# Performance work log

Hardware: AMD Instinct MI355X
Metric: run time of the kernel (lower is better)

## Reference

```python
import jax, jax.numpy as jnp
import numpy as np
from jax import lax

B, CODELEN, COMLEN, NAST, SUBG = 32, 50, 30, 300, 4
EMB, H, ASTHOPS = 300, 256, 2
AST_VOCAB, COM_VOCAB = 10000, 10000


def gru(x, h0, wih, whh, bih, bhh):
    # PyTorch GRU cell semantics. x: [N, T, D], h0: [N, H] -> (ys [N,T,H], hT [N,H])
    xg = jnp.einsum('ntd,gd->ntg', x, wih) + bih  # precompute input gates [N,T,3H]
    def step(h, xt):
        hg = h @ whh.T + bhh
        xr, xz, xn = jnp.split(xt, 3, axis=-1)
        hr, hz, hn = jnp.split(hg, 3, axis=-1)
        r = jax.nn.sigmoid(xr + hr)
        z = jax.nn.sigmoid(xz + hz)
        n = jnp.tanh(xn + r * hn)
        hnew = (1.0 - z) * n + z * h
        return hnew, hnew
    hT, ys = lax.scan(step, h0, jnp.swapaxes(xg, 0, 1))
    return jnp.swapaxes(ys, 0, 1), hT


def dot_attn(q, k):
    # DotProductAttention in eval mode (dropout = identity)
    scale = 1.0 / jnp.sqrt(jnp.asarray(q.shape[-1], q.dtype))
    s = jnp.einsum('bqd,bkd->bqk', q, k) * scale
    return jnp.einsum('bqk,bkd->bqd', jax.nn.softmax(s, axis=-1), k)


def setup_inputs() -> dict:
    key = jax.random.key(0)
    ks = jax.random.split(key, 32)
    def rn(k, shp, sc=0.05):
        return jax.random.normal(k, shp, jnp.float32) * sc
    inp = {}
    inp['x0'] = jax.random.randint(ks[0], (B, CODELEN), 0, AST_VOCAB)
    inp['x1'] = jax.random.randint(ks[1], (B, COMLEN), 0, COM_VOCAB)
    inp['x2'] = jax.random.randint(ks[2], (B, SUBG, NAST), 0, AST_VOCAB)
    inp['adj'] = jax.random.uniform(ks[3], (B, SUBG, NAST, NAST), jnp.float32) * (1.0 / NAST)
    inp['emb_ast'] = rn(ks[4], (AST_VOCAB, EMB), 0.5)
    inp['emb_com'] = rn(ks[5], (COM_VOCAB, EMB), 0.5)
    inp['gru1_wih'] = rn(ks[6], (3 * H, EMB)); inp['gru1_whh'] = rn(ks[7], (3 * H, H))
    inp['gru1_bih'] = rn(ks[8], (3 * H,));    inp['gru1_bhh'] = rn(ks[9], (3 * H,))
    inp['gru2_wih'] = rn(ks[10], (3 * H, EMB)); inp['gru2_whh'] = rn(ks[11], (3 * H, H))
    inp['gru2_bih'] = rn(ks[12], (3 * H,));     inp['gru2_bhh'] = rn(ks[13], (3 * H,))
    inp['gru4_wih'] = rn(ks[14], (3 * H, NAST * EMB), 0.01)
    inp['gru4_whh'] = rn(ks[15], (3 * H, H))
    inp['gru4_bih'] = rn(ks[16], (3 * H,)); inp['gru4_bhh'] = rn(ks[17], (3 * H,))
    inp['gru58_wih'] = rn(ks[18], (SUBG, 3 * H, EMB)); inp['gru58_whh'] = rn(ks[19], (SUBG, 3 * H, H))
    inp['gru58_bih'] = rn(ks[20], (SUBG, 3 * H));      inp['gru58_bhh'] = rn(ks[21], (SUBG, 3 * H))
    inp['gcn_w'] = rn(ks[22], (EMB, EMB)); inp['gcn_b'] = rn(ks[23], (EMB,))
    inp['dense_w'] = rn(ks[24], (H, 3 * H)); inp['dense_b'] = rn(ks[25], (H,))
    inp['lin_w'] = rn(ks[26], (COM_VOCAB, COMLEN * H), 0.01); inp['lin_b'] = rn(ks[27], (COM_VOCAB,))
    return inp


def reference(x0, x1, x2, adj, emb_ast, emb_com,
              gru1_wih, gru1_whh, gru1_bih, gru1_bhh,
              gru2_wih, gru2_whh, gru2_bih, gru2_bhh,
              gru4_wih, gru4_whh, gru4_bih, gru4_bhh,
              gru58_wih, gru58_whh, gru58_bih, gru58_bhh,
              gcn_w, gcn_b, dense_w, dense_b, lin_w, lin_b):
    b = x0.shape[0]
    scale = 1.0 / jnp.sqrt(jnp.float32(H))
    # token encoder + comment decoder
    tencout, tstate = gru(emb_ast[x0], jnp.zeros((b, H), jnp.float32),
                          gru1_wih, gru1_whh, gru1_bih, gru1_bhh)
    decout, _ = gru(emb_com[x1], tstate, gru2_wih, gru2_whh, gru2_bih, gru2_bhh)
    tcontext = dot_attn(decout, tencout)
    # GCN over 4 sub-graphs (torch code mutates astwork in place -> tmp alias sees post-GCN feats)
    astwork = jnp.transpose(emb_ast[x2], (1, 0, 2, 3))  # [4,B,N,300]
    adjp = jnp.transpose(adj, (1, 0, 2, 3))             # [4,B,N,N]
    for _ in range(ASTHOPS):
        support = jnp.einsum('sbnd,de->sbne', astwork, gcn_w)
        astwork = jax.nn.relu(jnp.einsum('sbnm,sbme->sbne', adjp, support) + gcn_b)
    # TimeDistributed(gru4): batch = 4 sub-graphs, sequence = B, input = flattened node feats
    g4in = astwork.reshape(SUBG, b, NAST * EMB)
    g4out, _ = gru(g4in, jnp.zeros((SUBG, H), jnp.float32),
                   gru4_wih, gru4_whh, gru4_bih, gru4_bhh)
    astw = jnp.transpose(g4out, (1, 0, 2))  # [B,4,H]
    ahier = jax.nn.softmax(jnp.einsum('bqd,bsd->bqs', decout, astw) * scale, axis=-1)
    ahier_p = jnp.transpose(ahier, (2, 0, 1))  # [4,B,Q]
    # per-sub-graph node GRUs (gru5..gru8) vmapped over the sub-graph axis
    outs, _ = jax.vmap(gru, in_axes=(0, None, 0, 0, 0, 0))(
        astwork, tstate, gru58_wih, gru58_whh, gru58_bih, gru58_bhh)  # [4,B,N,H]
    sc = jax.nn.softmax(jnp.einsum('bqd,sbkd->sbqk', decout, outs) * scale, axis=-1)
    new_atten = sc * ahier_p[:, :, :, None]  # element_wise_mul with hierarchy weights
    acontext = jnp.einsum('sbqk,sbkd->bqd', new_atten, outs)  # bmm then sum over sub-graphs
    acontext = dot_attn(decout, acontext)
    context = jnp.concatenate([tcontext, decout, acontext], axis=-1)  # [B,Q,768]
    out = jax.nn.relu(context @ dense_w.T + dense_b)
    out = out.reshape(b, -1)  # [B, 7680]
    return out @ lin_w.T + lin_b  # [B, comvocab]
```

## Files before the change

### kernel.cpp

```cpp
#include <hip/hip_runtime.h>
#include <hip/hip_fp16.h>
#include <hip/hip_bf16.h>


typedef __attribute__((ext_vector_type(8))) short  bf16x8;
typedef __attribute__((ext_vector_type(4))) float  f32x4;

__device__ inline unsigned short f2bs(float f) {
  __hip_bfloat16 h = __float2bfloat16(f);
  unsigned short u; __builtin_memcpy(&u, &h, 2); return u;
}
__device__ inline float bs2f(unsigned short u) {
  unsigned v = (unsigned)u << 16;
  float f; __builtin_memcpy(&f, &v, 4); return f;
}
__device__ inline float sigf(float x) { return 1.f / (1.f + __expf(-x)); }
__device__ inline float tanhf_(float x) {
  const float e = __expf(-2.f * fabsf(x));
  return copysignf((1.f - e) / (1.f + e), x);
}

template <bool ABF, bool BBF, int OUTM, bool RELU, bool GATHER = false, bool BKN = false>
__global__ __launch_bounds__(256) void k_mfma(
    const void* __restrict__ Av, long lda, long a_ss, long a_sb,
    const void* __restrict__ Bv, long ldb, long b_ss, long b_sb,
    void* __restrict__ Cv, long ldc, long c_ss, long c_sb,
    const float* __restrict__ bias, long bias_ss,
    const int* __restrict__ gidx,
    int M, int N, int K, int zb, int ksplit)
{
  __shared__ unsigned short As[128][40];
  __shared__ unsigned short Bs[128][40];
  const int tid = threadIdx.x;
  const int zi = blockIdx.z;
  const int bi = zi / ksplit;
  const int ks = zi - bi * ksplit;
  const int sIdx = bi / zb;
  const int bIdx = bi - sIdx * zb;
  const int row0 = blockIdx.y * 128;
  const int col0 = blockIdx.x * 128;
  const int Kc = ((K + ksplit * 32 - 1) / (ksplit * 32)) * 32;
  const int kbeg = ks * Kc;
  const int kend = min(K, kbeg + Kc);
  if (kbeg >= kend) return;

  const char* Ab = (const char*)Av + ((long)sIdx * a_ss + (long)bIdx * a_sb) * (ABF ? 2 : 4);
  const char* Bb = (const char*)Bv + ((long)sIdx * b_ss + (long)bIdx * b_sb) * (BBF ? 2 : 4);
  char* Cb = (char*)Cv + ((long)sIdx * c_ss + (long)bIdx * c_sb) * ((OUTM == 1 || OUTM == 3) ? 2 : 4);

  const int w = tid >> 6, l = tid & 63;
  const int wr = w >> 1, wc = w & 1;
  const int lr = l & 15, lg = l >> 4;

  f32x4 acc[4][4];
#pragma unroll
  for (int m = 0; m < 4; ++m)
#pragma unroll
    for (int n = 0; n < 4; ++n) acc[m][n] = f32x4{0.f, 0.f, 0.f, 0.f};

  const int sr = tid >> 1;
  const int sk = (tid & 1) * 16;

  for (int kt = kbeg; kt < kend; kt += 32) {
    {
      const int gr = row0 + sr;
      if (ABF) {
        const unsigned short* src = (const unsigned short*)(Ab + ((long)gr * lda + kt + sk) * 2);
        if (gr < M && kt + sk + 16 <= kend) {
          const uint2* p = (const uint2*)src;
          *(uint2*)&As[sr][sk + 0]  = p[0];
          *(uint2*)&As[sr][sk + 4]  = p[1];
          *(uint2*)&As[sr][sk + 8]  = p[2];
          *(uint2*)&As[sr][sk + 12] = p[3];
        } else {
#pragma unroll
          for (int i = 0; i < 16; ++i) {
            const int kk = kt + sk + i;
            As[sr][sk + i] = (gr < M && kk < kend) ? src[i] : (unsigned short)0;
          }
        }
      } else {
        const float* src;
        if (GATHER) src = (const float*)Av + ((gr < M) ? (long)gidx[gr] * lda : 0) + kt + sk;
        else        src = (const float*)(Ab + ((long)gr * lda + kt + sk) * 4);
        if (gr < M && kt + sk + 16 <= kend) {
#pragma unroll
          for (int q = 0; q < 4; ++q) {
            const float4 v = ((const float4*)src)[q];
            *(unsigned*)&As[sr][sk + q * 4 + 0] = (unsigned)f2bs(v.x) | ((unsigned)f2bs(v.y) << 16);
            *(unsigned*)&As[sr][sk + q * 4 + 2] = (unsigned)f2bs(v.z) | ((unsigned)f2bs(v.w) << 16);
          }
        } else {
#pragma unroll
          for (int i = 0; i < 16; ++i) {
            const int kk = kt + sk + i;
            As[sr][sk + i] = (gr < M && kk < kend) ? f2bs(src[i]) : (unsigned short)0;
          }
        }
      }
    }
    if (BKN) {
      const int kk = tid >> 3;
      const int cb = (tid & 7) * 16;
      const int gk = kt + kk;
#pragma unroll
      for (int q = 0; q < 16; ++q) {
        const int gc = col0 + cb + q;
        unsigned short v = 0;
        if (gk < kend && gc < N) {
          if (BBF) v = ((const unsigned short*)Bb)[(long)gk * ldb + gc];
          else     v = f2bs(((const float*)Bb)[(long)gk * ldb + gc]);
        }
        Bs[cb + q][kk] = v;
      }
    } else {
      const int gc = col0 + sr;
      if (BBF) {
        const unsigned short* src = (const unsigned short*)(Bb + ((long)gc * ldb + kt + sk) * 2);
        if (gc < N && kt + sk + 16 <= kend) {
          const uint2* p = (const uint2*)src;
          *(uint2*)&Bs[sr][sk + 0]  = p[0];
          *(uint2*)&Bs[sr][sk + 4]  = p[1];
          *(uint2*)&Bs[sr][sk + 8]  = p[2];
          *(uint2*)&Bs[sr][sk + 12] = p[3];
        } else {
#pragma unroll
          for (int i = 0; i < 16; ++i) {
            const int kk = kt + sk + i;
            Bs[sr][sk + i] = (gc < N && kk < kend) ? src[i] : (unsigned short)0;
          }
        }
      } else {
        const float* src = (const float*)(Bb + ((long)gc * ldb + kt + sk) * 4);
        if (gc < N && kt + sk + 16 <= kend) {
#pragma unroll
          for (int q = 0; q < 4; ++q) {
            const float4 v = ((const float4*)src)[q];
            *(unsigned*)&Bs[sr][sk + q * 4 + 0] = (unsigned)f2bs(v.x) | ((unsigned)f2bs(v.y) << 16);
            *(unsigned*)&Bs[sr][sk + q * 4 + 2] = (unsigned)f2bs(v.z) | ((unsigned)f2bs(v.w) << 16);
          }
        } else {
#pragma unroll
          for (int i = 0; i < 16; ++i) {
            const int kk = kt + sk + i;
            Bs[sr][sk + i] = (gc < N && kk < kend) ? f2bs(src[i]) : (unsigned short)0;
          }
        }
      }
    }
    __syncthreads();
    bf16x8 af[4], bf[4];
#pragma unroll
    for (int m = 0; m < 4; ++m)
      af[m] = *(const bf16x8*)&As[wr * 64 + m * 16 + lr][lg * 8];
#pragma unroll
    for (int n = 0; n < 4; ++n)
      bf[n] = *(const bf16x8*)&Bs[wc * 64 + n * 16 + lr][lg * 8];
#pragma unroll
    for (int m = 0; m < 4; ++m)
#pragma unroll
      for (int n = 0; n < 4; ++n)
        acc[m][n] = __builtin_amdgcn_mfma_f32_16x16x32_bf16(af[m], bf[n], acc[m][n], 0, 0, 0);
    __syncthreads();
  }

  const float* bp = bias ? bias + (long)sIdx * bias_ss : nullptr;
#pragma unroll
  for (int m = 0; m < 4; ++m) {
#pragma unroll
    for (int n = 0; n < 4; ++n) {
      const int col = col0 + wc * 64 + n * 16 + lr;
      const int rb  = row0 + wr * 64 + m * 16 + lg * 4;
      const f32x4 v = acc[m][n];
      if (col >= N) continue;
      if (OUTM == 3) {
        unsigned short* ct = (unsigned short*)Cb + (long)col * ldc + rb;
        if (rb + 4 <= M) {
          ushort4 pk;
          pk.x = f2bs(v[0]); pk.y = f2bs(v[1]); pk.z = f2bs(v[2]); pk.w = f2bs(v[3]);
          *(ushort4*)ct = pk;
        } else {
#pragma unroll
          for (int r = 0; r < 4; ++r) if (rb + r < M) ct[r] = f2bs(v[r]);
        }
      } else {
        const float bv = bp ? bp[col] : 0.f;
#pragma unroll
        for (int r = 0; r < 4; ++r) {
          const int row = rb + r;
          if (row >= M) continue;
          float x = v[r] + bv;
          if (RELU) x = fmaxf(x, 0.f);
          if (OUTM == 0) ((float*)Cb)[(long)row * ldc + col] = x;
          else if (OUTM == 1) ((unsigned short*)Cb)[(long)row * ldc + col] = f2bs(x);
          else atomicAdd((float*)Cb + (long)row * ldc + col, x);
        }
      }
    }
  }
}

template <bool XBF, bool YBF>
__global__ __launch_bounds__(1024, 1) void k_gru_v3(
    const void* __restrict__ xg,
    const float* __restrict__ h0, int h0_mod,
    const unsigned short* __restrict__ whh_bf, long w_stride, int cpw,
    const float* __restrict__ bhh, long b_stride,
    void* __restrict__ ys, float* __restrict__ hT, int T)
{
  const int c   = blockIdx.x;
  const int tid = threadIdx.x;
  const int wv  = tid >> 6;
  const int l   = tid & 63;
  const int lr  = l & 15;
  const int lg  = l >> 4;

  __shared__ unsigned short A_lds[8][64][8];
  __shared__ float gate_lds[772];
  __shared__ float bhh_lds[768];
  __shared__ float h_lds[256];
  __shared__ uint4 xbuf[2][192];

  const unsigned short* W = whh_bf + (long)(c / cpw) * w_stride;
  bf16x8 bfr[3][8];
#pragma unroll
  for (int nt = 0; nt < 3; ++nt) {
    const unsigned short* wp = W + (long)(wv * 48 + nt * 16 + lr) * 256 + lg * 8;
#pragma unroll
    for (int kt = 0; kt < 8; ++kt)
      bfr[nt][kt] = *(const bf16x8*)(wp + kt * 32);
  }
  if (tid < 768) bhh_lds[tid] = bhh[(long)(c / cpw) * b_stride + tid];
  {
    unsigned* az = (unsigned*)A_lds;
    for (int i = tid; i < 2048; i += 1024) az[i] = 0;
  }
  __syncthreads();

  if (tid < 32) {
    const int j0 = tid * 8;
    bf16x8 pk;
#pragma unroll
    for (int e = 0; e < 8; ++e) {
      const float hv = h0 ? h0[(long)(c % h0_mod) * 256 + j0 + e] : 0.f;
      h_lds[j0 + e] = hv;
      pk[e] = (short)f2bs(hv);
    }
    *(bf16x8*)&A_lds[j0 >> 5][((j0 >> 3) & 3) * 16][0] = pk;
  }
  const int esz = XBF ? 2 : 4;
  const int xlanes = XBF ? 96 : 192;
  const char* xbase = (const char*)xg + (long)c * T * 768 * esz;
  if (tid < xlanes) xbuf[0][tid] = *(const uint4*)(xbase + tid * 16);
  __syncthreads();

  int cur = 0;
  for (int t = 0; t < T; ++t) {
    uint4 xs = uint4{0, 0, 0, 0};
    const bool xact = (tid < xlanes) && (t + 1 < T);
    if (xact) xs = *(const uint4*)(xbase + (long)(t + 1) * 768 * esz + tid * 16);

    f32x4 acc[3];
    acc[0] = f32x4{0.f, 0.f, 0.f, 0.f};
    acc[1] = f32x4{0.f, 0.f, 0.f, 0.f};
    acc[2] = f32x4{0.f, 0.f, 0.f, 0.f};
#pragma unroll
    for (int kt = 0; kt < 8; ++kt) {
      const bf16x8 af = *(const bf16x8*)&A_lds[kt][l][0];
#pragma unroll
      for (int nt = 0; nt < 3; ++nt)
        acc[nt] = __builtin_amdgcn_mfma_f32_16x16x32_bf16(af, bfr[nt][kt], acc[nt], 0, 0, 0);
    }
    if (lg == 0) {
#pragma unroll
      for (int nt = 0; nt < 3; ++nt)
        gate_lds[wv * 48 + nt * 16 + lr] = acc[nt][0];
    }
    __syncthreads();

    if (xact) xbuf[cur ^ 1][tid] = xs;

    if (tid < 32) {
      const int j0 = tid * 8;
      float hn[8];
#pragma unroll
      for (int e = 0; e < 8; ++e) {
        const int u = j0 + e;
        float xr, xz, xn;
        if (XBF) {
          const unsigned short* xp = (const unsigned short*)&xbuf[cur][0];
          xr = bs2f(xp[u]); xz = bs2f(xp[256 + u]); xn = bs2f(xp[512 + u]);
        } else {
          const float* xp = (const float*)&xbuf[cur][0];
          xr = xp[u]; xz = xp[256 + u]; xn = xp[512 + u];
        }
        const float rr = sigf(xr + gate_lds[u] + bhh_lds[u]);
        const float zz = sigf(xz + gate_lds[256 + u] + bhh_lds[256 + u]);
        const float nv = tanhf_(xn + rr * (gate_lds[512 + u] + bhh_lds[512 + u]));
        hn[e] = (1.f - zz) * nv + zz * h_lds[u];
      }
      bf16x8 pk;
#pragma unroll
      for (int e = 0; e < 8; ++e) {
        h_lds[j0 + e] = hn[e];
        pk[e] = (short)f2bs(hn[e]);
      }
      *(bf16x8*)&A_lds[j0 >> 5][((j0 >> 3) & 3) * 16][0] = pk;
      if (ys) {
        if (YBF) {
          unsigned short* yp = (unsigned short*)ys + ((long)c * T + t) * 256 + j0;
          *(bf16x8*)yp = pk;
        } else {
          float* yp = (float*)ys + ((long)c * T + t) * 256 + j0;
          *(float4*)yp = float4{hn[0], hn[1], hn[2], hn[3]};
          *(float4*)(yp + 4) = float4{hn[4], hn[5], hn[6], hn[7]};
        }
      }
    }
    __syncthreads();
    cur ^= 1;
  }
  if (hT && tid < 32) {
    const int j0 = tid * 8;
    float* hp = hT + (long)c * 256 + j0;
#pragma unroll
    for (int e = 0; e < 8; ++e) hp[e] = h_lds[j0 + e];
  }
}

__global__ __launch_bounds__(256) void k_init_bias(
    float* __restrict__ C, const float* __restrict__ bias, int M, int N)
{
  const int total = M * N;
  for (int i = blockIdx.x * 256 + threadIdx.x; i < total; i += gridDim.x * 256)
    C[i] = bias[i % N];
}

__global__ __launch_bounds__(256) void k_gather_ast(
    const float* __restrict__ emb, const int* __restrict__ x2,
    unsigned short* __restrict__ outp)
{
  const int total = 4 * 32 * 300 * 300;
  for (int idx = blockIdx.x * 256 + threadIdx.x; idx < total; idx += gridDim.x * 256) {
    const int d = idx % 300;
    const int r = idx / 300;
    const int n = r % 300;
    const int r2 = r / 300;
    const int b = r2 % 32;
    const int s = r2 / 32;
    outp[idx] = f2bs(emb[(long)x2[(b * 4 + s) * 300 + n] * 300 + d]);
  }
}

__global__ __launch_bounds__(256) void k_twb(
    const float* __restrict__ w, unsigned short* __restrict__ o, int R, int C)
{
  const int total = R * C;
  for (int i = blockIdx.x * 256 + threadIdx.x; i < total; i += gridDim.x * 256) {
    const int r = i / C, c = i - r * C;
    o[(long)c * R + r] = f2bs(w[i]);
  }
}

__global__ __launch_bounds__(256) void k_f2b(
    const float* __restrict__ a, unsigned short* __restrict__ o, int n)
{
  for (int i = blockIdx.x * 256 + threadIdx.x; i < n; i += gridDim.x * 256)
    o[i] = f2bs(a[i]);
}

__global__ __launch_bounds__(256) void k_attn(
    const float* __restrict__ q, const float* __restrict__ kv,
    float* __restrict__ out, int Q, int L)
{
  const int bq = blockIdx.x;
  const int b = bq / Q;
  const int tid = threadIdx.x;
  const int g = tid >> 3, l = tid & 7;
  __shared__ float qv[256];
  __shared__ float sc[64];
  qv[tid] = q[(long)bq * 256 + tid];
  __syncthreads();
  for (int k0 = 0; k0 < L; k0 += 32) {
    const int k = k0 + g;
    float s = 0.f;
    if (k < L) {
      const float* kr = kv + ((long)b * L + k) * 256;
      for (int d = l; d < 256; d += 8) s += qv[d] * kr[d];
    }
    s += __shfl_xor(s, 1);
    s += __shfl_xor(s, 2);
    s += __shfl_xor(s, 4);
    if (k < L && l == 0) sc[k] = s * 0.0625f;
  }
  __syncthreads();
  float m = -1e30f;
  for (int k = 0; k < L; ++k) m = fmaxf(m, sc[k]);
  float den = 0.f;
  for (int k = 0; k < L; ++k) den += __expf(sc[k] - m);
  __syncthreads();
  if (tid < L) sc[tid] = __expf(sc[tid] - m);
  __syncthreads();
  const float* kb = kv + (long)b * L * 256;
  float acc = 0.f;
  for (int k = 0; k < L; ++k) acc += sc[k] * kb[(long)k * 256 + tid];
  out[(long)bq * 256 + tid] = acc / den;
}

__global__ __launch_bounds__(64) void k_hier(
    const float* __restrict__ dec, const float* __restrict__ g4out,
    float* __restrict__ ahier, int Q)
{
  const int bq = blockIdx.x;
  const int b = bq / Q;
  const int l = threadIdx.x;
  float s[4] = {0.f, 0.f, 0.f, 0.f};
#pragma unroll
  for (int i = 0; i < 4; ++i) {
    const int d = l * 4 + i;
    const float qd = dec[(long)bq * 256 + d];
#pragma unroll
    for (int sg = 0; sg < 4; ++sg)
      s[sg] += qd * g4out[((long)sg * 32 + b) * 256 + d];
  }
#pragma unroll
  for (int off = 32; off >= 1; off >>= 1)
#pragma unroll
    for (int sg = 0; sg < 4; ++sg) s[sg] += __shfl_xor(s[sg], off);
  if (l == 0) {
    float m = -1e30f;
#pragma unroll
    for (int sg = 0; sg < 4; ++sg) m = fmaxf(m, s[sg] * 0.0625f);
    float e[4], den = 0.f;
#pragma unroll
    for (int sg = 0; sg < 4; ++sg) { e[sg] = __expf(s[sg] * 0.0625f - m); den += e[sg]; }
#pragma unroll
    for (int sg = 0; sg < 4; ++sg) ahier[(long)bq * 4 + sg] = e[sg] / den;
  }
}

__global__ __launch_bounds__(64) void k_smax(
    float* __restrict__ sc, const float* __restrict__ ahier)
{
  const int id = blockIdx.x;
  const int s = id / 960;
  const int bq = id - s * 960;
  float* row = sc + (long)id * 300;
  const int l = threadIdx.x;
  float v[5];
  float m = -1e30f;
#pragma unroll
  for (int i = 0; i < 5; ++i) {
    const int k = l + i * 64;
    v[i] = (k < 300) ? row[k] * 0.0625f : -1e30f;
    m = fmaxf(m, v[i]);
  }
#pragma unroll
  for (int off = 32; off >= 1; off >>= 1) m = fmaxf(m, __shfl_xor(m, off));
  float den = 0.f;
#pragma unroll
  for (int i = 0; i < 5; ++i) { v[i] = __expf(v[i] - m); den += v[i]; }
#pragma unroll
  for (int off = 32; off >= 1; off >>= 1) den += __shfl_xor(den, off);
  const float w = ahier[(long)bq * 4 + s] / den;
#pragma unroll
  for (int i = 0; i < 5; ++i) {
    const int k = l + i * 64;
    if (k < 300) row[k] = v[i] * w;
  }
}

__global__ __launch_bounds__(256) void k_concat(
    const float* __restrict__ a, const float* __restrict__ b,
    const float* __restrict__ c, float* __restrict__ out, int rows)
{
  const int total = rows * 768;
  for (int i = blockIdx.x * 256 + threadIdx.x; i < total; i += gridDim.x * 256) {
    const int r = i / 768, col = i - r * 768;
    float v;
    if (col < 256) v = a[(long)r * 256 + col];
    else if (col < 512) v = b[(long)r * 256 + col - 256];
    else v = c[(long)r * 256 + col - 512];
    out[i] = v;
  }
}

extern "C" void kernel_launch(void* const* d_in, const int* in_sizes, int n_in,
                              void* d_out, int out_size, void* d_ws, size_t ws_size,
                              hipStream_t stream) {
  const int*   x0      = (const int*)d_in[0];
  const int*   x1      = (const int*)d_in[1];
  const int*   x2      = (const int*)d_in[2];
  const float* adj     = (const float*)d_in[3];
  const float* emb_ast = (const float*)d_in[4];
  const float* emb_com = (const float*)d_in[5];
  const float* g1_wih  = (const float*)d_in[6];
  const float* g1_whh  = (const float*)d_in[7];
  const float* g1_bih  = (const float*)d_in[8];
  const float* g1_bhh  = (const float*)d_in[9];
  const float* g2_wih  = (const float*)d_in[10];
  const float* g2_whh  = (const float*)d_in[11];
  const float* g2_bih  = (const float*)d_in[12];
  const float* g2_bhh  = (const float*)d_in[13];
  const float* g4_wih  = (const float*)d_in[14];
  const float* g4_whh  = (const float*)d_in[15];
  const float* g4_bih  = (const float*)d_in[16];
  const float* g4_bhh  = (const float*)d_in[17];
  const float* g58_wih = (const float*)d_in[18];
  const float* g58_whh = (const float*)d_in[19];
  const float* g58_bih = (const float*)d_in[20];
  const float* g58_bhh = (const float*)d_in[21];
  const float* gcn_w   = (const float*)d_in[22];
  const float* gcn_b   = (const float*)d_in[23];
  const float* dw      = (const float*)d_in[24];
  const float* db      = (const float*)d_in[25];
  const float* lw      = (const float*)d_in[26];
  const float* lb      = (const float*)d_in[27];
  float* out = (float*)d_out;
  float* ws  = (float*)d_ws;

  unsigned short* astwork_bf = (unsigned short*)ws;
  unsigned short* supportT   = (unsigned short*)(ws + 5760000L);
  unsigned short* g58xg_bf   = (unsigned short*)(ws + 11520000L);
  unsigned short* outsb_bf   = (unsigned short*)(ws + 26265600L);
  unsigned short* xg1_bf     = (unsigned short*)(ws + 31180800L);
  unsigned short* xg2_bf     = (unsigned short*)(ws + 31795200L);
  float* tenc    = ws + 32163840L;
  float* tstate  = ws + 32573440L;
  float* dec     = ws + 32581632L;
  float* tctx    = ws + 32827392L;
  float* g4xg    = ws + 33073152L;
  float* g4out   = ws + 33171456L;
  float* ahier   = ws + 33204224L;
  float* actx1   = ws + 33208064L;
  float* actx    = ws + 33453824L;
  float* dense   = ws + 33699584L;
  float* ctmp    = ws + 33945344L;
  float* scbuf   = ws + 34682624L;
  unsigned short* gcn_wT    = (unsigned short*)(ws + 35834624L);
  unsigned short* dense_bf  = (unsigned short*)(ws + 35879624L);
  unsigned short* g1whh_bf  = (unsigned short*)(ws + 36002504L);
  unsigned short* g2whh_bf  = (unsigned short*)(ws + 36100808L);
  unsigned short* g4whh_bf  = (unsigned short*)(ws + 36199112L);
  unsigned short* g58whh_bf = (unsigned short*)(ws + 36297416L);

  const dim3 blk(256);

  k_gather_ast<<<dim3(4096), blk, 0, stream>>>(emb_ast, x2, astwork_bf);
  k_twb<<<dim3(90), blk, 0, stream>>>(gcn_w, gcn_wT, 300, 300);
  k_f2b<<<dim3(192), blk, 0, stream>>>(g1_whh, g1whh_bf, 196608);
  k_f2b<<<dim3(192), blk, 0, stream>>>(g2_whh, g2whh_bf, 196608);
  k_f2b<<<dim3(192), blk, 0, stream>>>(g4_whh, g4whh_bf, 196608);
  k_f2b<<<dim3(768), blk, 0, stream>>>(g58_whh, g58whh_bf, 786432);

  for (int hop = 0; hop < 2; ++hop) {
    k_mfma<true, true, 3, false><<<dim3(3, 3, 128), blk, 0, stream>>>(
        astwork_bf, 300, 2880000, 90000,
        gcn_wT, 300, 0, 0,
        supportT, 300, 2880000, 90000,
        nullptr, 0, nullptr, 300, 300, 300, 32, 1);
    k_mfma<false, true, 1, true><<<dim3(3, 3, 128), blk, 0, stream>>>(
        adj, 300, 90000, 360000,
        supportT, 300, 2880000, 90000,
        astwork_bf, 300, 2880000, 90000,
        gcn_b, 0, nullptr, 300, 300, 300, 32, 1);
  }

  k_mfma<false, false, 1, false, true><<<dim3(6, 13, 1), blk, 0, stream>>>(
      emb_ast, 300, 0, 0, g1_wih, 300, 0, 0, xg1_bf, 768, 0, 0,
      g1_bih, 0, x0, 1600, 768, 300, 1, 1);
  k_gru_v3<true, false><<<dim3(32), dim3(1024), 0, stream>>>(
      xg1_bf, nullptr, 1, g1whh_bf, 0, 32, g1_bhh, 0, tenc, tstate, 50);

  k_mfma<false, false, 1, false, true><<<dim3(6, 8, 1), blk, 0, stream>>>(
      emb_com, 300, 0, 0, g2_wih, 300, 0, 0, xg2_bf, 768, 0, 0,
      g2_bih, 0, x1, 960, 768, 300, 1, 1);
  k_gru_v3<true, false><<<dim3(32), dim3(1024), 0, stream>>>(
      xg2_bf, tstate, 32, g2whh_bf, 0, 32, g2_bhh, 0, dec, nullptr, 30);

  k_attn<<<dim3(960), blk, 0, stream>>>(dec, tenc, tctx, 30, 50);

  k_init_bias<<<dim3(384), blk, 0, stream>>>(g4xg, g4_bih, 128, 768);
  k_mfma<true, false, 2, false><<<dim3(6, 1, 43), blk, 0, stream>>>(
      astwork_bf, 90000, 0, 0, g4_wih, 90000, 0, 0, g4xg, 768, 0, 0,
      nullptr, 0, nullptr, 128, 768, 90000, 1, 43);
  k_gru_v3<false, false><<<dim3(4), dim3(1024), 0, stream>>>(
      g4xg, nullptr, 1, g4whh_bf, 0, 4, g4_bhh, 0, g4out, nullptr, 32);

  k_hier<<<dim3(960), dim3(64), 0, stream>>>(dec, g4out, ahier, 30);

  k_mfma<true, false, 1, false><<<dim3(6, 75, 4), blk, 0, stream>>>(
      astwork_bf, 300, 2880000, 0, g58_wih, 300, 230400, 0,
      g58xg_bf, 768, 7372800, 0, g58_bih, 768, nullptr, 9600, 768, 300, 1, 1);
  k_gru_v3<true, true><<<dim3(128), dim3(1024), 0, stream>>>(
      g58xg_bf, tstate, 32, g58whh_bf, 196608, 32, g58_bhh, 768,
      outsb_bf, nullptr, 300);

  k_mfma<false, true, 0, false><<<dim3(3, 1, 128), blk, 0, stream>>>(
      dec, 256, 0, 7680, outsb_bf, 256, 2457600, 76800, scbuf, 300, 288000, 9000,
      nullptr, 0, nullptr, 30, 300, 256, 32, 1);
  k_smax<<<dim3(3840), dim3(64), 0, stream>>>(scbuf, ahier);
  hipMemsetAsync(actx1, 0, 245760 * sizeof(float), stream);
  k_mfma<false, true, 2, false, false, true><<<dim3(2, 1, 128), blk, 0, stream>>>(
      scbuf, 300, 288000, 9000, outsb_bf, 256, 2457600, 76800, actx1, 256, 0, 7680,
      nullptr, 0, nullptr, 30, 256, 300, 32, 1);

  k_attn<<<dim3(960), blk, 0, stream>>>(dec, actx1, actx, 30, 30);

  k_concat<<<dim3(2880), blk, 0, stream>>>(tctx, dec, actx, ctmp, 960);
  k_mfma<false, false, 0, true><<<dim3(2, 8, 1), blk, 0, stream>>>(
      ctmp, 768, 0, 0, dw, 768, 0, 0, dense, 256, 0, 0,
      db, 0, nullptr, 960, 256, 768, 1, 1);
  k_f2b<<<dim3(960), blk, 0, stream>>>(dense, dense_bf, 245760);

  k_init_bias<<<dim3(1250), blk, 0, stream>>>(out, lb, 32, 10000);
  k_mfma<true, false, 2, false><<<dim3(79, 1, 6), blk, 0, stream>>>(
      dense_bf, 7680, 0, 0, lw, 7680, 0, 0, out, 10000, 0, 0,
      nullptr, 0, nullptr, 32, 10000, 7680, 1, 6);
}
```

Baseline: 1.893 ms.

## Batch multiple GRU chains per block and pre-convert adjacency to bf16

The GRU recurrence kernel now handles several independent sequences per block. They are stacked as rows of the MFMA A-operand, so one set of register-resident recurrent weights serves up to 16 chains at once, and the hidden state is kept in registers with double-buffered LDS. This cuts the grid from one block per sequence to a few blocks and replaces the near-empty 1-row MFMAs with fuller ones. It also reduces the per-step work of the single-thread-group gate update. Separately, the adjacency matrix is converted to bf16 once and then used in the GCN hops, which adds a conversion pass in exchange for halving A-operand traffic.

After: 2.303 ms. 21.6% more time.

```diff
diff --git a/kernel.cpp b/kernel.cpp
--- a/kernel.cpp
+++ b/kernel.cpp
@@ -200,131 +200,163 @@
   }
 }
 
-template <bool XBF, bool YBF>
-__global__ __launch_bounds__(1024, 1) void k_gru_v3(
+template <int CPB, bool XBF, bool YBF>
+__global__ __launch_bounds__(512) void k_gru_v4(
     const void* __restrict__ xg,
     const float* __restrict__ h0, int h0_mod,
     const unsigned short* __restrict__ whh_bf, long w_stride, int cpw,
     const float* __restrict__ bhh, long b_stride,
     void* __restrict__ ys, float* __restrict__ hT, int T)
 {
-  const int c   = blockIdx.x;
+  constexpr int ESZ  = XBF ? 2 : 4;
+  constexpr int VPR  = 768 * ESZ / 16;
+  constexpr int XVEC = CPB * VPR;
+  constexpr int NQ   = (XVEC + 511) / 512;
+
   const int tid = threadIdx.x;
+  const int c0  = blockIdx.x * CPB;
   const int wv  = tid >> 6;
   const int l   = tid & 63;
   const int lr  = l & 15;
   const int lg  = l >> 4;
 
-  __shared__ unsigned short A_lds[8][64][8];
-  __shared__ float gate_lds[772];
+  __shared__ unsigned short A_lds[2][8][64][8];
+  __shared__ float gate_lds[CPB][772];
   __shared__ float bhh_lds[768];
-  __shared__ float h_lds[256];
-  __shared__ uint4 xbuf[2][192];
-
-  const unsigned short* W = whh_bf + (long)(c / cpw) * w_stride;
-  bf16x8 bfr[3][8];
-#pragma unroll
-  for (int nt = 0; nt < 3; ++nt) {
-    const unsigned short* wp = W + (long)(wv * 48 + nt * 16 + lr) * 256 + lg * 8;
-#pragma unroll
-    for (int kt = 0; kt < 8; ++kt)
-      bfr[nt][kt] = *(const bf16x8*)(wp + kt * 32);
-  }
-  if (tid < 768) bhh_lds[tid] = bhh[(long)(c / cpw) * b_stride + tid];
-  {
-    unsigned* az = (unsigned*)A_lds;
-    for (int i = tid; i < 2048; i += 1024) az[i] = 0;
-  }
+  __shared__ uint4 xbuf[2][XVEC];
+
+  { unsigned* az = (unsigned*)A_lds;
+    for (int i = tid; i < 4096; i += 512) az[i] = 0; }
   __syncthreads();
 
-  if (tid < 32) {
-    const int j0 = tid * 8;
+  const unsigned short* W = whh_bf + (long)(c0 / cpw) * w_stride;
+  bf16x8 bfr[6][8];
+#pragma unroll
+  for (int nt = 0; nt < 6; ++nt) {
+    const unsigned short* wp = W + (long)(wv * 96 + nt * 16 + lr) * 256 + lg * 8;
+#pragma unroll
+    for (int kt = 0; kt < 8; ++kt) bfr[nt][kt] = *(const bf16x8*)(wp + kt * 32);
+  }
+  for (int i = tid; i < 768; i += 512)
+    bhh_lds[i] = bhh[(long)(c0 / cpw) * b_stride + i];
+
+  const int c   = tid >> 5;
+  const int jb  = tid & 31;
+  const bool act = c < CPB;
+  const int u0  = jb * 8;
+
+  float h[8];
+  if (act) {
+#pragma unroll
+    for (int e = 0; e < 8; ++e)
+      h[e] = h0 ? h0[(long)((c0 + c) % h0_mod) * 256 + u0 + e] : 0.f;
     bf16x8 pk;
 #pragma unroll
-    for (int e = 0; e < 8; ++e) {
-      const float hv = h0 ? h0[(long)(c % h0_mod) * 256 + j0 + e] : 0.f;
-      h_lds[j0 + e] = hv;
-      pk[e] = (short)f2bs(hv);
-    }
-    *(bf16x8*)&A_lds[j0 >> 5][((j0 >> 3) & 3) * 16][0] = pk;
-  }
-  const int esz = XBF ? 2 : 4;
-  const int xlanes = XBF ? 96 : 192;
-  const char* xbase = (const char*)xg + (long)c * T * 768 * esz;
-  if (tid < xlanes) xbuf[0][tid] = *(const uint4*)(xbase + tid * 16);
+    for (int e = 0; e < 8; ++e) pk[e] = (short)f2bs(h[e]);
+    *(bf16x8*)&A_lds[0][jb >> 2][(jb & 3) * 16 + c][0] = pk;
+  }
+
+  const char* xbase = (const char*)xg + (long)c0 * T * 768 * ESZ;
+  long poff[NQ]; bool pact[NQ];
+#pragma unroll
+  for (int q = 0; q < NQ; ++q) {
+    const int i = tid + q * 512;
+    pact[q] = i < XVEC;
+    const int ci = pact[q] ? i / VPR : 0;
+    const int of = i - ci * VPR;
+    poff[q] = (long)ci * T * 768 * ESZ + (long)of * 16;
+  }
+#pragma unroll
+  for (int q = 0; q < NQ; ++q)
+    if (pact[q]) ((uint4*)xbuf[0])[tid + q * 512] = *(const uint4*)(xbase + poff[q]);
   __syncthreads();
 
   int cur = 0;
   for (int t = 0; t < T; ++t) {
-    uint4 xs = uint4{0, 0, 0, 0};
-    const bool xact = (tid < xlanes) && (t + 1 < T);
-    if (xact) xs = *(const uint4*)(xbase + (long)(t + 1) * 768 * esz + tid * 16);
-
-    f32x4 acc[3];
-    acc[0] = f32x4{0.f, 0.f, 0.f, 0.f};
-    acc[1] = f32x4{0.f, 0.f, 0.f, 0.f};
-    acc[2] = f32x4{0.f, 0.f, 0.f, 0.f};
+    uint4 xs[NQ];
+    const bool pf = (t + 1 < T);
+    if (pf) {
+#pragma unroll
+      for (int q = 0; q < NQ; ++q)
+        if (pact[q]) xs[q] = *(const uint4*)(xbase + poff[q] + (long)(t + 1) * 768 * ESZ);
+    }
+
+    f32x4 acc[6];
+#pragma unroll
+    for (int nt = 0; nt < 6; ++nt) acc[nt] = f32x4{0.f, 0.f, 0.f, 0.f};
 #pragma unroll
     for (int kt = 0; kt < 8; ++kt) {
-      const bf16x8 af = *(const bf16x8*)&A_lds[kt][l][0];
-#pragma unroll
-      for (int nt = 0; nt < 3; ++nt)
+      const bf16x8 af = *(const bf16x8*)&A_lds[cur][kt][l][0];
+#pragma unroll
+      for (int nt = 0; nt < 6; ++nt)
         acc[nt] = __builtin_amdgcn_mfma_f32_16x16x32_bf16(af, bfr[nt][kt], acc[nt], 0, 0, 0);
     }
-    if (lg == 0) {
-#pragma unroll
-      for (int nt = 0; nt < 3; ++nt)
-        gate_lds[wv * 48 + nt * 16 + lr] = acc[nt][0];
+    if (lg * 4 < CPB) {
+#pragma unroll
+      for (int nt = 0; nt < 6; ++nt) {
+        const int col = wv * 96 + nt * 16 + lr;
+#pragma unroll
+        for (int r = 0; r < 4; ++r) gate_lds[lg * 4 + r][col] = acc[nt][r];
+      }
     }
     __syncthreads();
 
-    if (xact) xbuf[cur ^ 1][tid] = xs;
-
-    if (tid < 32) {
-      const int j0 = tid * 8;
-      float hn[8];
+    if (pf) {
+#pragma unroll
+      for (int q = 0; q < NQ; ++q)
+        if (pact[q]) ((uint4*)xbuf[cur ^ 1])[tid + q * 512] = xs[q];
+    }
+
+    if (act) {
+      float xr[8], xz[8], xn[8];
+      if (XBF) {
+        const unsigned short* xp = (const unsigned short*)xbuf[cur] + c * 768;
+        const bf16x8 vr = *(const bf16x8*)(xp + u0);
+        const bf16x8 vz = *(const bf16x8*)(xp + 256 + u0);
+        const bf16x8 vn = *(const bf16x8*)(xp + 512 + u0);
+#pragma unroll
+        for (int e = 0; e < 8; ++e) {
+          xr[e] = bs2f((unsigned short)vr[e]);
+          xz[e] = bs2f((unsigned short)vz[e]);
+          xn[e] = bs2f((unsigned short)vn[e]);
+        }
+      } else {
+        const float* xp = (const float*)xbuf[cur] + c * 768;
+        *(float4*)&xr[0] = *(const float4*)(xp + u0);
+        *(float4*)&xr[4] = *(const float4*)(xp + u0 + 4);
+        *(float4*)&xz[0] = *(const float4*)(xp + 256 + u0);
+        *(float4*)&xz[4] = *(const float4*)(xp + 256 + u0 + 4);
+        *(float4*)&xn[0] = *(const float4*)(xp + 512 + u0);
+        *(float4*)&xn[4] = *(const float4*)(xp + 512 + u0 + 4);
+      }
+      bf16x8 pk;
 #pragma unroll
       for (int e = 0; e < 8; ++e) {
-        const int u = j0 + e;
-        float xr, xz, xn;
-        if (XBF) {
-          const unsigned short* xp = (const unsigned short*)&xbuf[cur][0];
-          xr = bs2f(xp[u]); xz = bs2f(xp[256 + u]); xn = bs2f(xp[512 + u]);
-        } else {
-          const float* xp = (const float*)&xbuf[cur][0];
-          xr = xp[u]; xz = xp[256 + u]; xn = xp[512 + u];
-        }
-        const float rr = sigf(xr + gate_lds[u] + bhh_lds[u]);
-        const float zz = sigf(xz + gate_lds[256 + u] + bhh_lds[256 + u]);
-        const float nv = tanhf_(xn + rr * (gate_lds[512 + u] + bhh_lds[512 + u]));
-        hn[e] = (1.f - zz) * nv + zz * h_lds[u];
-      }
-      bf16x8 pk;
-#pragma unroll
-      for (int e = 0; e < 8; ++e) {
-        h_lds[j0 + e] = hn[e];
-        pk[e] = (short)f2bs(hn[e]);
-      }
-      *(bf16x8*)&A_lds[j0 >> 5][((j0 >> 3) & 3) * 16][0] = pk;
+        const int u = u0 + e;
+        const float rr = sigf(xr[e] + gate_lds[c][u] + bhh_lds[u]);
+        const float zz = sigf(xz[e] + gate_lds[c][256 + u] + bhh_lds[256 + u]);
+        const float nv = tanhf_(xn[e] + rr * (gate_lds[c][512 + u] + bhh_lds[512 + u]));
+        h[e] = (1.f - zz) * nv + zz * h[e];
+        pk[e] = (short)f2bs(h[e]);
+      }
+      *(bf16x8*)&A_lds[cur ^ 1][jb >> 2][(jb & 3) * 16 + c][0] = pk;
       if (ys) {
         if (YBF) {
-          unsigned short* yp = (unsigned short*)ys + ((long)c * T + t) * 256 + j0;
-          *(bf16x8*)yp = pk;
+          *(bf16x8*)((unsigned short*)ys + ((long)(c0 + c) * T + t) * 256 + u0) = pk;
         } else {
-          float* yp = (float*)ys + ((long)c * T + t) * 256 + j0;
-          *(float4*)yp = float4{hn[0], hn[1], hn[2], hn[3]};
-          *(float4*)(yp + 4) = float4{hn[4], hn[5], hn[6], hn[7]};
+          float* yp = (float*)ys + ((long)(c0 + c) * T + t) * 256 + u0;
+          *(float4*)yp = float4{h[0], h[1], h[2], h[3]};
+          *(float4*)(yp + 4) = float4{h[4], h[5], h[6], h[7]};
         }
       }
     }
     __syncthreads();
     cur ^= 1;
   }
-  if (hT && tid < 32) {
-    const int j0 = tid * 8;
-    float* hp = hT + (long)c * 256 + j0;
-#pragma unroll
-    for (int e = 0; e < 8; ++e) hp[e] = h_lds[j0 + e];
+  if (hT && act) {
+    float* hp = hT + (long)(c0 + c) * 256 + u0;
+    *(float4*)hp = float4{h[0], h[1], h[2], h[3]};
+    *(float4*)(hp + 4) = float4{h[4], h[5], h[6], h[7]};
   }
 }
 
@@ -543,6 +575,7 @@
   unsigned short* g2whh_bf  = (unsigned short*)(ws + 36100808L);
   unsigned short* g4whh_bf  = (unsigned short*)(ws + 36199112L);
   unsigned short* g58whh_bf = (unsigned short*)(ws + 36297416L);
+  unsigned short* adj_bf    = (unsigned short*)(ws + 36690632L);
 
   const dim3 blk(256);
 
@@ -552,6 +585,7 @@
   k_f2b<<<dim3(192), blk, 0, stream>>>(g2_whh, g2whh_bf, 196608);
   k_f2b<<<dim3(192), blk, 0, stream>>>(g4_whh, g4whh_bf, 196608);
   k_f2b<<<dim3(768), blk, 0, stream>>>(g58_whh, g58whh_bf, 786432);
+  k_f2b<<<dim3(4096), blk, 0, stream>>>(adj, adj_bf, 11520000);
 
   for (int hop = 0; hop < 2; ++hop) {
     k_mfma<true, true, 3, false><<<dim3(3, 3, 128), blk, 0, stream>>>(
@@ -559,8 +593,8 @@
         gcn_wT, 300, 0, 0,
         supportT, 300, 2880000, 90000,
         nullptr, 0, nullptr, 300, 300, 300, 32, 1);
-    k_mfma<false, true, 1, true><<<dim3(3, 3, 128), blk, 0, stream>>>(
-        adj, 300, 90000, 360000,
+    k_mfma<true, true, 1, true><<<dim3(3, 3, 128), blk, 0, stream>>>(
+        adj_bf, 300, 90000, 360000,
         supportT, 300, 2880000, 90000,
         astwork_bf, 300, 2880000, 90000,
         gcn_b, 0, nullptr, 300, 300, 300, 32, 1);
@@ -569,13 +603,13 @@
   k_mfma<false, false, 1, false, true><<<dim3(6, 13, 1), blk, 0, stream>>>(
       emb_ast, 300, 0, 0, g1_wih, 300, 0, 0, xg1_bf, 768, 0, 0,
       g1_bih, 0, x0, 1600, 768, 300, 1, 1);
-  k_gru_v3<true, false><<<dim3(32), dim3(1024), 0, stream>>>(
+  k_gru_v4<16, true, false><<<dim3(2), dim3(512), 0, stream>>>(
       xg1_bf, nullptr, 1, g1whh_bf, 0, 32, g1_bhh, 0, tenc, tstate, 50);
 
   k_mfma<false, false, 1, false, true><<<dim3(6, 8, 1), blk, 0, stream>>>(
       emb_com, 300, 0, 0, g2_wih, 300, 0, 0, xg2_bf, 768, 0, 0,
       g2_bih, 0, x1, 960, 768, 300, 1, 1);
-  k_gru_v3<true, false><<<dim3(32), dim3(1024), 0, stream>>>(
+  k_gru_v4<16, true, false><<<dim3(2), dim3(512), 0, stream>>>(
       xg2_bf, tstate, 32, g2whh_bf, 0, 32, g2_bhh, 0, dec, nullptr, 30);
 
   k_attn<<<dim3(960), blk, 0, stream>>>(dec, tenc, tctx, 30, 50);
@@ -584,7 +618,7 @@
   k_mfma<true, false, 2, false><<<dim3(6, 1, 43), blk, 0, stream>>>(
       astwork_bf, 90000, 0, 0, g4_wih, 90000, 0, 0, g4xg, 768, 0, 0,
       nullptr, 0, nullptr, 128, 768, 90000, 1, 43);
-  k_gru_v3<false, false><<<dim3(4), dim3(1024), 0, stream>>>(
+  k_gru_v4<4, false, false><<<dim3(1), dim3(512), 0, stream>>>(
       g4xg, nullptr, 1, g4whh_bf, 0, 4, g4_bhh, 0, g4out, nullptr, 32);
 
   k_hier<<<dim3(960), dim3(64), 0, stream>>>(dec, g4out, ahier, 30);
@@ -592,7 +626,7 @@
   k_mfma<true, false, 1, false><<<dim3(6, 75, 4), blk, 0, stream>>>(
       astwork_bf, 300, 2880000, 0, g58_wih, 300, 230400, 0,
       g58xg_bf, 768, 7372800, 0, g58_bih, 768, nullptr, 9600, 768, 300, 1, 1);
-  k_gru_v3<true, true><<<dim3(128), dim3(1024), 0, stream>>>(
+  k_gru_v4<8, true, true><<<dim3(16), dim3(512), 0, stream>>>(
       g58xg_bf, tstate, 32, g58whh_bf, 196608, 32, g58_bhh, 768,
       outsb_bf, nullptr, 300);
 
```
